# Kernel tuning notes

Hardware: AMD Instinct MI355X
Metric: run time of the kernel (lower is better)

The kernel has to match this reference:

```python
import jax, jax.numpy as jnp
import numpy as np

NUM_HEADS = 8
N_WIN = 7
TOPK = 4


def _grid2seq(x, rs, m):
    # x: (B, C, H, W) -> (B, m, nregion, reg_size, head_dim)
    B, C, H, W = x.shape
    rh, rw = H // rs[0], W // rs[1]
    d = C // m
    x = x.reshape(B, m, d, rh, rs[0], rw, rs[1])
    x = jnp.einsum('bmdhpwq->bmhwpqd', x).reshape(B, m, rh * rw, rs[0] * rs[1], d)
    return x, rh, rw


def _seq2grid(x, rh, rw, rs):
    B, m, nreg, rsq, d = x.shape
    x = x.reshape(B, m, rh, rw, rs[0], rs[1], d)
    return jnp.einsum('bmhwpqd->bmdhpwq', x).reshape(B, m * d, rh * rs[0], rw * rs[1])


def setup_inputs() -> dict:
    key = jax.random.key(0)
    ks = jax.random.split(key, 7)
    C = 256
    inp = {
        'x': jax.random.normal(ks[0], (16, C, 56, 56), jnp.float32),
        'w_qkv': jax.random.normal(ks[1], (3 * C, C), jnp.float32) * 0.02,
        'b_qkv': jax.random.normal(ks[2], (3 * C,), jnp.float32) * 0.02,
        'w_lepe': jax.random.normal(ks[3], (C, 1, 3, 3), jnp.float32) * 0.02,
        'b_lepe': jax.random.normal(ks[4], (C,), jnp.float32) * 0.02,
        'w_out': jax.random.normal(ks[5], (C, C), jnp.float32) * 0.02,
        'b_out': jax.random.normal(ks[6], (C,), jnp.float32) * 0.02,
    }
    return inp


def reference(x, w_qkv, b_qkv, w_lepe, b_lepe, w_out, b_out):
    N, C, H, W = x.shape
    m = NUM_HEADS
    d = C // m
    scale = d ** (-0.5)
    rs = (max(1, H // N_WIN), max(1, W // N_WIN))  # (8, 8) here; H,W divisible -> no pad
    rh, rw = H // rs[0], W // rs[1]

    # 1x1 conv qkv projection
    qkv = jnp.einsum('nchw,oc->nohw', x, w_qkv) + b_qkv[None, :, None, None]
    q, k, v = jnp.split(qkv, 3, axis=1)

    # region-level routing (avg_pool over each region; exact divisibility -> plain mean)
    def region_mean(t):
        return t.reshape(N, C, rh, rs[0], rw, rs[1]).mean(axis=(3, 5))  # (N,C,rh,rw)

    q_r = jax.lax.stop_gradient(region_mean(q)).reshape(N, C, rh * rw).transpose(0, 2, 1)  # (N,nreg,C)
    k_r = jax.lax.stop_gradient(region_mean(k)).reshape(N, C, rh * rw)  # (N,C,nreg)
    a_r = q_r @ k_r  # (N, nreg, nreg)
    k_fixed = min(TOPK, a_r.shape[-1])
    _, idx_r = jax.lax.top_k(a_r, k_fixed)  # (N, nreg, topk)
    idx_r = jnp.broadcast_to(idx_r[:, None], (N, m, rh * rw, k_fixed))  # (N,m,nreg,topk)

    # token-level attention within routed regions
    q_seq, _, _ = _grid2seq(q, rs, m)  # (N,m,nreg,rs2,d)
    k_seq, _, _ = _grid2seq(k, rs, m)
    v_seq, _, _ = _grid2seq(v, rs, m)
    rs2 = k_seq.shape[-2]

    gather = jax.vmap(jax.vmap(lambda seq, i: seq[i]))  # over (batch, head)
    key_g = gather(k_seq, idx_r).reshape(N, m, rh * rw, k_fixed * rs2, d)
    val_g = gather(v_seq, idx_r).reshape(N, m, rh * rw, k_fixed * rs2, d)

    attn = jax.nn.softmax(jnp.einsum('bmnpd,bmnkd->bmnpk', q_seq * scale, key_g), axis=-1)
    out = jnp.einsum('bmnpk,bmnkd->bmnpd', attn, val_g)
    out = _seq2grid(out, rh, rw, rs)  # (N, C, H, W)

    # LEPE: depthwise 3x3 conv on v
    lepe = jax.lax.conv_general_dilated(
        v, w_lepe, window_strides=(1, 1), padding='SAME',
        feature_group_count=C, dimension_numbers=('NCHW', 'OIHW', 'NCHW'))
    out = out + lepe + b_lepe[None, :, None, None]

    # 1x1 conv output projection
    out = jnp.einsum('nchw,oc->nohw', out, w_out) + b_out[None, :, None, None]
    return out
```

## Files before the change

kernel.cpp:

```cpp
#include <hip/hip_runtime.h>
#include <cstdint>

#define DEV __device__ __forceinline__

using short8 = __attribute__((ext_vector_type(8))) short;
using f32x4  = __attribute__((ext_vector_type(4))) float;

#define MFMA __builtin_amdgcn_mfma_f32_16x16x32_bf16

DEV float bf2f(unsigned short u){
  union { unsigned int i; float f; } v; v.i = ((unsigned int)u) << 16; return v.f;
}
DEV unsigned short f2bf(float f){
  union { float f; unsigned int i; } v; v.f = f;
  unsigned int x = v.i;
  return (unsigned short)((x + 0x7fffu + ((x >> 16) & 1u)) >> 16);
}
DEV unsigned int cvtpk(float a, float b){
  unsigned int r;
  asm("v_cvt_pk_bf16_f32 %0, %1, %2" : "=v"(r) : "v"(a), "v"(b));
  return r;
}

__global__ __launch_bounds__(256) void k_prep(const float* __restrict__ w_qkv,
                                              const float* __restrict__ w_out,
                                              unsigned short* __restrict__ wqh_t,
                                              unsigned short* __restrict__ woh_t,
                                              unsigned short* __restrict__ wol_t){
  int i = blockIdx.x*256 + threadIdx.x;
  if (i < 196608){
    int o = i >> 8, c = i & 255, kc = c >> 5, kk = c & 31;
    wqh_t[kc*24576 + o*32 + kk] = f2bf(w_qkv[i]);
  } else {
    int j = i - 196608;
    if (j < 65536){
      int o = j >> 8, c = j & 255, kc = c >> 5, kk = c & 31;
      float v = w_out[j];
      unsigned short h = f2bf(v);
      int dst = kc*8192 + o*32 + kk;
      woh_t[dst] = h;
      wol_t[dst] = f2bf(v - bf2f(h));
    }
  }
}

__global__ __launch_bounds__(256) void k_xbar(const float* __restrict__ x,
                                              float* __restrict__ xbar){
  const int ry = blockIdx.x, n = blockIdx.y, cz = blockIdx.z;
  const int t = threadIdx.x, cg = t>>6, lane = t&63;
  for (int ci = 0; ci < 16; ++ci){
    int c = cz*64 + ci*4 + cg;
    const float* base = x + ((size_t)n*256 + c)*3136 + ry*8*56;
    float acc = 0.f;
    if (lane < 56){
      #pragma unroll
      for (int yy = 0; yy < 8; ++yy) acc += base[yy*56 + lane];
    }
    acc += __shfl_xor(acc, 1, 64);
    acc += __shfl_xor(acc, 2, 64);
    acc += __shfl_xor(acc, 4, 64);
    if ((lane&7) == 0 && lane < 56)
      xbar[((size_t)n*49 + ry*7 + (lane>>3))*256 + c] = acc * (1.0f/64.0f);
  }
}

__global__ __launch_bounds__(256) void k_qrkr(const float* __restrict__ xbar,
                                              const float* __restrict__ w_qkv,
                                              const float* __restrict__ b_qkv,
                                              float* __restrict__ q_r,
                                              float* __restrict__ k_r){
  __shared__ float4 xb4[448];
  const int wb = blockIdx.x, n = blockIdx.y, rz = blockIdx.z, t = threadIdx.x;
  {
    const float4* src = (const float4*)(xbar + (size_t)n*12544) + rz*448;
    for (int i = t; i < 448; i += 256) xb4[i] = src[i];
  }
  const int wrow = wb*64 + (t>>2), kl = t&3;
  float4 wreg[16];
  {
    const float4* wsrc = (const float4*)(w_qkv + (size_t)wrow*256) + kl*16;
    #pragma unroll
    for (int i = 0; i < 16; ++i) wreg[i] = wsrc[i];
  }
  __syncthreads();
  const float bias = b_qkv[wrow];
  for (int rl = 0; rl < 7; ++rl){
    float s = 0.f;
    #pragma unroll
    for (int i = 0; i < 16; ++i){
      float4 a = wreg[i], b = xb4[rl*64 + kl*16 + i];
      s += a.x*b.x + a.y*b.y + a.z*b.z + a.w*b.w;
    }
    s += __shfl_xor(s, 1, 64);
    s += __shfl_xor(s, 2, 64);
    if (kl == 0){
      int reg = rz*7 + rl;
      if (wrow < 256) q_r[((size_t)n*49 + reg)*256 + wrow] = s + bias;
      else            k_r[((size_t)n*49 + reg)*256 + wrow - 256] = s + bias;
    }
  }
}

__global__ __launch_bounds__(64) void k_topk(const float* __restrict__ q_r,
                                             const float* __restrict__ k_r,
                                             int* __restrict__ idx){
  __shared__ float sc[49];
  const int qreg = blockIdx.x, n = blockIdx.y, l = threadIdx.x;
  const float* qrow = q_r + ((size_t)n*49 + qreg)*256;
  const float q0 = qrow[l], q1 = qrow[l+64], q2 = qrow[l+128], q3 = qrow[l+192];
  for (int kr = 0; kr < 49; ++kr){
    const float* krow = k_r + ((size_t)n*49 + kr)*256;
    float s = q0*krow[l] + q1*krow[l+64] + q2*krow[l+128] + q3*krow[l+192];
    #pragma unroll
    for (int m = 1; m < 64; m <<= 1) s += __shfl_xor(s, m, 64);
    if (l == 0) sc[kr] = s;
  }
  __syncthreads();
  if (l == 0){
    #pragma unroll
    for (int s = 0; s < 4; ++s){
      float best = -3.4e38f; int bi = 0;
      for (int kr = 0; kr < 49; ++kr) if (sc[kr] > best){ best = sc[kr]; bi = kr; }
      idx[((size_t)n*49 + qreg)*4 + s] = bi;
      sc[bi] = -3.4e38f;
    }
  }
}

__global__ __launch_bounds__(256) void k_qkv(const float* __restrict__ x,
                                             const unsigned short* __restrict__ wqh_t,
                                             const float* __restrict__ b_qkv,
                                             unsigned short* __restrict__ q_rm,
                                             unsigned short* __restrict__ k_rm,
                                             unsigned short* __restrict__ v_t){
  __shared__ unsigned short xl[64*256];
  const int lin = blockIdx.x;
  const int xcd = lin & 7, jj = lin >> 3;
  const int jobid = xcd*294 + jj;
  const int z = jobid % 3;
  const int pair = jobid / 3;
  const int reg = pair % 49, n = pair / 49;

  const int ry = reg/7, rx = reg%7;
  const int t = threadIdx.x, w = t>>6, g = (t>>4)&3, c16 = t&15;
  {
    const int pq = (t & 15)*4, cc = t >> 4;
    const int row = pq >> 3, col = pq & 7;
    const float* src = x + ((size_t)n*256 + cc)*3136 + (ry*8 + row)*56 + rx*8 + col;
    for (int ci = 0; ci < 16; ++ci){
      float4 v4 = *reinterpret_cast<const float4*>(src + (size_t)ci*16*3136);
      int c = ci*16 + cc;
      xl[((pq+0)*256 + c) ^ (((pq+0)&15)<<3)] = f2bf(v4.x);
      xl[((pq+1)*256 + c) ^ (((pq+1)&15)<<3)] = f2bf(v4.y);
      xl[((pq+2)*256 + c) ^ (((pq+2)&15)<<3)] = f2bf(v4.z);
      xl[((pq+3)*256 + c) ^ (((pq+3)&15)<<3)] = f2bf(v4.w);
    }
  }
  __syncthreads();
  const size_t rb = (size_t)(n*8)*49 + reg;
  const int osw = w*16;

  if (z < 2){
    f32x4 acc[4][4] = {};
    for (int kc = 0; kc < 8; ++kc){
      short8 xf[4];
      #pragma unroll
      for (int pt = 0; pt < 4; ++pt){
        int p = pt*16 + c16;
        xf[pt] = *reinterpret_cast<const short8*>(&xl[(p*256 + kc*32 + 8*g) ^ ((p&15)<<3)]);
      }
      #pragma unroll
      for (int oi = 0; oi < 4; ++oi){
        const int os = z*256 + oi*64 + osw;
        short8 wf = *reinterpret_cast<const short8*>(wqh_t + (size_t)kc*24576 + (os + c16)*32 + 8*g);
        #pragma unroll
        for (int pt = 0; pt < 4; ++pt)
          acc[oi][pt] = MFMA(xf[pt], wf, acc[oi][pt], 0, 0, 0);
      }
    }
    #pragma unroll
    for (int oi = 0; oi < 4; ++oi){
      const int o = z*256 + oi*64 + osw + c16;
      const float bias = b_qkv[o];
      const int oc = o & 255, hh = oc >> 5, dd = oc & 31;
      unsigned short* dst = ((z == 0) ? q_rm : k_rm) + (rb + hh*49)*2048 + dd;
      #pragma unroll
      for (int pt = 0; pt < 4; ++pt)
        #pragma unroll
        for (int r = 0; r < 4; ++r){
          int tok = pt*16 + 4*g + r;
          dst[tok*32] = f2bf(acc[oi][pt][r] + bias);
        }
    }
  } else {
    f32x4 acc[4][4] = {};
    for (int kc = 0; kc < 8; ++kc){
      short8 xf[4];
      #pragma unroll
      for (int pt = 0; pt < 4; ++pt){
        int p = pt*16 + c16;
        xf[pt] = *reinterpret_cast<const short8*>(&xl[(p*256 + kc*32 + 8*g) ^ ((p&15)<<3)]);
      }
      #pragma unroll
      for (int oi = 0; oi < 4; ++oi){
        const int os = oi*64 + osw;
        short8 wf = *reinterpret_cast<const short8*>(wqh_t + (size_t)kc*24576 + (512 + os + c16)*32 + 8*g);
        #pragma unroll
        for (int pt = 0; pt < 4; ++pt)
          acc[oi][pt] = MFMA(wf, xf[pt], acc[oi][pt], 0, 0, 0);
      }
    }
    #pragma unroll
    for (int oi = 0; oi < 4; ++oi){
      #pragma unroll
      for (int r = 0; r < 4; ++r){
        int c = oi*64 + osw + 4*g + r;
        const float bias = b_qkv[512 + c];
        int hh = c >> 5, ch = c & 31;
        unsigned short* dst = v_t + (rb + hh*49)*2048 + ch*32;
        #pragma unroll
        for (int pt = 0; pt < 4; ++pt){
          int tok = pt*16 + c16;
          dst[(tok>>5)*1024 + (tok&31)] = f2bf(acc[oi][pt][r] + bias);
        }
      }
    }
  }
}

__global__ __launch_bounds__(256, 4) void k_attn(const unsigned short* __restrict__ q_rm,
                                                 const unsigned short* __restrict__ k_rm,
                                                 const unsigned short* __restrict__ v_t,
                                                 const int* __restrict__ idx,
                                                 const float* __restrict__ w_lepe,
                                                 const float* __restrict__ b_lepe,
                                                 unsigned short* __restrict__ att_hi,
                                                 unsigned short* __restrict__ att_lo){
  __shared__ unsigned short Pw[4*2048];
  __shared__ unsigned short halo[10*320];
  __shared__ float wl_s[288];
  __shared__ float bl_s[32];

  const int lin = blockIdx.x + 49*(blockIdx.y + 8*blockIdx.z);
  const int xcd = lin & 7, j = lin >> 3;
  const int jq = j / 49;
  const int qreg = j - jq*49;
  const int hn = jq*8 + xcd;
  const int h = hn & 7, n = hn >> 3;

  const int t = threadIdx.x, w = t>>6, g = (t>>4)&3, c16 = t&15;
  const int ry = qreg/7, rx = qreg%7;
  const int gy0 = ry*8;

  int4 ridx = *reinterpret_cast<const int4*>(idx + ((size_t)n*49 + qreg)*4);
  int regs[4] = {ridx.x, ridx.y, ridx.z, ridx.w};

  const size_t hb = ((size_t)(n*8 + h))*49;

  wl_s[t < 288 ? t : 0] = w_lepe[h*288 + (t < 288 ? t : 0)];
  if (t < 32){
    wl_s[256 + t] = w_lepe[h*288 + 256 + t];
    bl_s[t] = b_lepe[h*32 + t];
  }
  #pragma unroll
  for (int pass = 0; pass < 2; ++pass){
    int s = pass ? (256 + t) : t;
    if (pass == 0 || t < 64){
      const int dy = s >> 5, c = s & 31;
      const int yy = gy0 + dy - 1;
      short8 inner = {0,0,0,0,0,0,0,0};
      unsigned short eL = 0, eR = 0;
      if (yy >= 0 && yy < 56){
        const int iry = yy >> 3, y7 = yy & 7;
        const size_t rowb = (size_t)(y7>>2)*1024 + c*32 + (y7&3)*8;
        inner = *reinterpret_cast<const short8*>(v_t + (hb + iry*7 + rx)*2048 + rowb);
        if (rx > 0) eL = v_t[(hb + iry*7 + rx - 1)*2048 + rowb + 7];
        if (rx < 6) eR = v_t[(hb + iry*7 + rx + 1)*2048 + rowb];
      }
      unsigned short* drow = &halo[dy*320 + c*10];
      drow[0] = eL;
      #pragma unroll
      for (int jj2 = 0; jj2 < 8; ++jj2) drow[1 + jj2] = (unsigned short)inner[jj2];
      drow[9] = eR;
    }
  }

  const int qtok = w*16 + c16;
  short8 qf = *reinterpret_cast<const short8*>(q_rm + (hb + qreg)*2048 + qtok*32 + 8*g);

  f32x4 s_acc[16];
  #pragma unroll
  for (int f = 0; f < 16; ++f){
    const int tt = (f&3)*16 + c16;
    short8 kf = *reinterpret_cast<const short8*>(
        k_rm + (hb + regs[f>>2])*2048 + tt*32 + 8*g);
    f32x4 z = {0.f, 0.f, 0.f, 0.f};
    s_acc[f] = MFMA(qf, kf, z, 0, 0, 0);
  }

  const float scale2 = 0.1767766952966369f * 1.4426950408889634f;
  float inv[4];
  #pragma unroll
  for (int r = 0; r < 4; ++r){
    float m = -3.4e38f;
    #pragma unroll
    for (int f = 0; f < 16; ++f) m = fmaxf(m, s_acc[f][r]);
    #pragma unroll
    for (int d = 1; d < 16; d <<= 1) m = fmaxf(m, __shfl_xor(m, d, 64));
    const float nms = -m*scale2;
    float su = 0.f;
    #pragma unroll
    for (int f = 0; f < 16; ++f){
      float e = exp2f(fmaf(s_acc[f][r], scale2, nms));
      s_acc[f][r] = e; su += e;
    }
    #pragma unroll
    for (int d = 1; d < 16; d <<= 1) su += __shfl_xor(su, d, 64);
    inv[r] = __builtin_amdgcn_rcpf(su);
  }

  f32x4 oacc[2] = {};
  unsigned short* wb2 = &Pw[w*2048];
  #pragma unroll
  for (int h2 = 0; h2 < 2; ++h2){
    #pragma unroll
    for (int r = 0; r < 4; ++r){
      int q = 4*g + r;
      #pragma unroll
      for (int f2 = 0; f2 < 8; f2 += 2){
        unsigned int pk = cvtpk(s_acc[8*h2 + f2][r], s_acc[8*h2 + f2 + 1][r]);
        wb2[(q*128 + f2*16 + c16) ^ ((q&7)<<3)]     = (unsigned short)pk;
        wb2[(q*128 + (f2+1)*16 + c16) ^ ((q&7)<<3)] = (unsigned short)(pk >> 16);
      }
    }
    asm volatile("s_waitcnt lgkmcnt(0)" ::: "memory");
    __builtin_amdgcn_sched_barrier(0);
    #pragma unroll
    for (int tcl = 0; tcl < 4; ++tcl){
      const int tc = 4*h2 + tcl;
      short8 pf = *reinterpret_cast<const short8*>(&wb2[(c16*128 + tcl*32 + 8*g) ^ ((c16&7)<<3)]);
      const size_t vb = (hb + regs[tc>>1])*2048 + (tc&1)*1024 + 8*g;
      #pragma unroll
      for (int dt = 0; dt < 2; ++dt){
        short8 vf = *reinterpret_cast<const short8*>(v_t + vb + (dt*16 + c16)*32);
        oacc[dt] = MFMA(pf, vf, oacc[dt], 0, 0, 0);
      }
    }
  }

  __syncthreads();
  const int tok0 = w*16 + 4*g;
  const int ty = tok0>>3, tx0 = tok0&7;
  #pragma unroll
  for (int dt = 0; dt < 2; ++dt){
    const int cl = dt*16 + c16;
    float wl[9];
    #pragma unroll
    for (int kk = 0; kk < 9; ++kk) wl[kk] = wl_s[cl*9 + kk];
    const float bl = bl_s[cl];
    float vwin[3][6];
    #pragma unroll
    for (int dy = 0; dy < 3; ++dy){
      const unsigned short* hrow = &halo[(ty+dy)*320 + cl*10 + tx0];
      #pragma unroll
      for (int jj = 0; jj < 6; ++jj)
        vwin[dy][jj] = bf2f(hrow[jj]);
    }
    #pragma unroll
    for (int r = 0; r < 4; ++r){
      float a = fmaf(oacc[dt][r], inv[r], bl);
      #pragma unroll
      for (int dy = 0; dy < 3; ++dy)
        #pragma unroll
        for (int dx = 0; dx < 3; ++dx)
          a += wl[dy*3 + dx] * vwin[dy][r + dx];
      int tok = tok0 + r;
      size_t o = ((size_t)(n*49 + qreg)*8 + h)*2048 + tok*32 + dt*16 + c16;
      unsigned short hi = (unsigned short)cvtpk(a, a);
      att_hi[o] = hi;
      float alo = a - bf2f(hi);
      att_lo[o] = (unsigned short)cvtpk(alo, alo);
    }
  }
}

__global__ __launch_bounds__(512) void k_oproj(const unsigned short* __restrict__ ah_,
                                               const unsigned short* __restrict__ al_,
                                               const unsigned short* __restrict__ wh_t,
                                               const unsigned short* __restrict__ wl_t,
                                               const float* __restrict__ b_out,
                                               float* __restrict__ out){
  const int reg = blockIdx.x, n = blockIdx.y;
  const int t = threadIdx.x, w8 = t>>6, g = (t>>4)&3, c16 = t&15;
  const int ry = reg/7, rx = reg%7;
  const size_t abase = ((size_t)(n*49 + reg))*8*2048;
  const int os1 = w8*16, os2 = os1 + 128;
  f32x4 acc[2][4] = {};
  for (int kc = 0; kc < 8; ++kc){
    const size_t wb = (size_t)kc*8192 + 8*g;
    short8 wh1 = *reinterpret_cast<const short8*>(wh_t + wb + (os1 + c16)*32);
    short8 wl1 = *reinterpret_cast<const short8*>(wl_t + wb + (os1 + c16)*32);
    short8 wh2 = *reinterpret_cast<const short8*>(wh_t + wb + (os2 + c16)*32);
    short8 wl2 = *reinterpret_cast<const short8*>(wl_t + wb + (os2 + c16)*32);
    #pragma unroll
    for (int pt = 0; pt < 4; ++pt){
      size_t off = abase + (size_t)kc*2048 + (pt*16 + c16)*32 + 8*g;
      short8 xh = *reinterpret_cast<const short8*>(ah_ + off);
      short8 xl = *reinterpret_cast<const short8*>(al_ + off);
      acc[0][pt] = MFMA(wh1, xh, acc[0][pt], 0, 0, 0);
      acc[0][pt] = MFMA(wh1, xl, acc[0][pt], 0, 0, 0);
      acc[0][pt] = MFMA(wl1, xh, acc[0][pt], 0, 0, 0);
      acc[1][pt] = MFMA(wh2, xh, acc[1][pt], 0, 0, 0);
      acc[1][pt] = MFMA(wh2, xl, acc[1][pt], 0, 0, 0);
      acc[1][pt] = MFMA(wl2, xh, acc[1][pt], 0, 0, 0);
    }
  }
  #pragma unroll
  for (int s = 0; s < 2; ++s){
    const int os = s ? os2 : os1;
    #pragma unroll
    for (int r = 0; r < 4; ++r){
      int o = os + 4*g + r;
      float bias = b_out[o];
      #pragma unroll
      for (int pt = 0; pt < 4; ++pt){
        int tok = pt*16 + c16;
        int p = (ry*8 + (tok>>3))*56 + rx*8 + (tok&7);
        out[((size_t)n*256 + o)*3136 + p] = acc[s][pt][r] + bias;
      }
    }
  }
}

extern "C" void kernel_launch(void* const* d_in, const int* in_sizes, int n_in,
                              void* d_out, int out_size, void* d_ws, size_t ws_size,
                              hipStream_t stream){
  const float* x      = (const float*)d_in[0];
  const float* w_qkv  = (const float*)d_in[1];
  const float* b_qkv  = (const float*)d_in[2];
  const float* w_lepe = (const float*)d_in[3];
  const float* b_lepe = (const float*)d_in[4];
  const float* w_out  = (const float*)d_in[5];
  const float* b_out  = (const float*)d_in[6];
  float* out = (float*)d_out;

  char* ws = (char*)d_ws;
  size_t off = 0;
  auto take = [&](size_t bytes)->char*{
    char* p = ws + off; off += (bytes + 255) & ~(size_t)255; return p;
  };
  const size_t TEN = (size_t)16*3136*256*2;
  unsigned short* q_rm   = (unsigned short*)take(TEN);
  unsigned short* k_rm   = (unsigned short*)take(TEN);
  unsigned short* v_t    = (unsigned short*)take(TEN);
  unsigned short* att_hi = (unsigned short*)take(TEN);
  unsigned short* att_lo = (unsigned short*)take(TEN);
  float* xbar = (float*)take((size_t)16*49*256*4);
  float* q_r  = (float*)take((size_t)16*49*256*4);
  float* k_r  = (float*)take((size_t)16*49*256*4);
  int*   idxb = (int*)take((size_t)16*49*4*4);
  unsigned short* wqh_t = (unsigned short*)take((size_t)768*256*2);
  unsigned short* woh_t = (unsigned short*)take((size_t)256*256*2);
  unsigned short* wol_t = (unsigned short*)take((size_t)256*256*2);

  k_prep <<<dim3(1024), 256, 0, stream>>>(w_qkv, w_out, wqh_t, woh_t, wol_t);
  k_xbar <<<dim3(7, 16, 4), 256, 0, stream>>>(x, xbar);
  k_qrkr <<<dim3(8, 16, 7), 256, 0, stream>>>(xbar, w_qkv, b_qkv, q_r, k_r);
  k_topk <<<dim3(49, 16), 64, 0, stream>>>(q_r, k_r, idxb);
  k_qkv  <<<dim3(2352), 256, 0, stream>>>(x, wqh_t, b_qkv, q_rm, k_rm, v_t);
  k_attn <<<dim3(49, 8, 16), 256, 0, stream>>>(q_rm, k_rm, v_t, idxb, w_lepe, b_lepe, att_hi, att_lo);
  k_oproj<<<dim3(49, 16), 512, 0, stream>>>(att_hi, att_lo, woh_t, wol_t, b_out, out);
}
```

Before: 253.0 us.

## Transpose QK^T MFMA and pass P through cross-lane shuffles instead of LDS

Swaps the MFMA operands so each lane holds scores for a single query row, which reduces the softmax max/sum reductions to two cross-lane shuffles per lane. The probabilities are then repacked into the A-operand layout of the PV MFMA with bpermute-style shuffles and selects, removing the per-wave LDS staging buffer and its waitcnt barriers. This cuts LDS use, which could raise occupancy. In exchange it adds many shuffle instructions and extra shuffles to redistribute the reciprocal sums.

Measured after the change: 250.4 us. About the same (-1.0%).

```diff
diff --git a/kernel.cpp b/kernel.cpp
--- a/kernel.cpp
+++ b/kernel.cpp
@@ -236,7 +236,6 @@
                                                  const float* __restrict__ b_lepe,
                                                  unsigned short* __restrict__ att_hi,
                                                  unsigned short* __restrict__ att_lo){
-  __shared__ unsigned short Pw[4*2048];
   __shared__ unsigned short halo[10*320];
   __shared__ float wl_s[288];
   __shared__ float bl_s[32];
@@ -295,58 +294,62 @@
     short8 kf = *reinterpret_cast<const short8*>(
         k_rm + (hb + regs[f>>2])*2048 + tt*32 + 8*g);
     f32x4 z = {0.f, 0.f, 0.f, 0.f};
-    s_acc[f] = MFMA(qf, kf, z, 0, 0, 0);
+    s_acc[f] = MFMA(kf, qf, z, 0, 0, 0);
   }
 
   const float scale2 = 0.1767766952966369f * 1.4426950408889634f;
-  float inv[4];
-  #pragma unroll
-  for (int r = 0; r < 4; ++r){
-    float m = -3.4e38f;
-    #pragma unroll
-    for (int f = 0; f < 16; ++f) m = fmaxf(m, s_acc[f][r]);
-    #pragma unroll
-    for (int d = 1; d < 16; d <<= 1) m = fmaxf(m, __shfl_xor(m, d, 64));
-    const float nms = -m*scale2;
-    float su = 0.f;
-    #pragma unroll
-    for (int f = 0; f < 16; ++f){
+  float m = -3.4e38f;
+  #pragma unroll
+  for (int f = 0; f < 16; ++f)
+    #pragma unroll
+    for (int r = 0; r < 4; ++r) m = fmaxf(m, s_acc[f][r]);
+  m = fmaxf(m, __shfl_xor(m, 16, 64));
+  m = fmaxf(m, __shfl_xor(m, 32, 64));
+  const float nms = -m*scale2;
+  float su = 0.f;
+  #pragma unroll
+  for (int f = 0; f < 16; ++f)
+    #pragma unroll
+    for (int r = 0; r < 4; ++r){
       float e = exp2f(fmaf(s_acc[f][r], scale2, nms));
       s_acc[f][r] = e; su += e;
     }
-    #pragma unroll
-    for (int d = 1; d < 16; d <<= 1) su += __shfl_xor(su, d, 64);
-    inv[r] = __builtin_amdgcn_rcpf(su);
-  }
+  su += __shfl_xor(su, 16, 64);
+  su += __shfl_xor(su, 32, 64);
+  const float inv_lane = __builtin_amdgcn_rcpf(su);
 
   f32x4 oacc[2] = {};
-  unsigned short* wb2 = &Pw[w*2048];
-  #pragma unroll
-  for (int h2 = 0; h2 < 2; ++h2){
-    #pragma unroll
-    for (int r = 0; r < 4; ++r){
-      int q = 4*g + r;
-      #pragma unroll
-      for (int f2 = 0; f2 < 8; f2 += 2){
-        unsigned int pk = cvtpk(s_acc[8*h2 + f2][r], s_acc[8*h2 + f2 + 1][r]);
-        wb2[(q*128 + f2*16 + c16) ^ ((q&7)<<3)]     = (unsigned short)pk;
-        wb2[(q*128 + (f2+1)*16 + c16) ^ ((q&7)<<3)] = (unsigned short)(pk >> 16);
-      }
-    }
-    asm volatile("s_waitcnt lgkmcnt(0)" ::: "memory");
-    __builtin_amdgcn_sched_barrier(0);
-    #pragma unroll
-    for (int tcl = 0; tcl < 4; ++tcl){
-      const int tc = 4*h2 + tcl;
-      short8 pf = *reinterpret_cast<const short8*>(&wb2[(c16*128 + tcl*32 + 8*g) ^ ((c16&7)<<3)]);
-      const size_t vb = (hb + regs[tc>>1])*2048 + (tc&1)*1024 + 8*g;
-      #pragma unroll
-      for (int dt = 0; dt < 2; ++dt){
-        short8 vf = *reinterpret_cast<const short8*>(v_t + vb + (dt*16 + c16)*32);
-        oacc[dt] = MFMA(pf, vf, oacc[dt], 0, 0, 0);
-      }
-    }
-  }
+  const int srcA = (t & 15) | ((t & 16) << 1);
+  const int srcB = srcA + 16;
+  const bool gsel = (t & 32) != 0;
+  #pragma unroll
+  for (int tc = 0; tc < 8; ++tc){
+    const int fb = (tc>>1)*4 + (tc&1)*2;
+    unsigned int a0 = cvtpk(s_acc[fb][0],   s_acc[fb][1]);
+    unsigned int a1 = cvtpk(s_acc[fb][2],   s_acc[fb][3]);
+    unsigned int b0 = cvtpk(s_acc[fb+1][0], s_acc[fb+1][1]);
+    unsigned int b1 = cvtpk(s_acc[fb+1][2], s_acc[fb+1][3]);
+    unsigned int wa0 = __shfl((int)a0, srcA, 64), wa1 = __shfl((int)a1, srcA, 64);
+    unsigned int wa2 = __shfl((int)a0, srcB, 64), wa3 = __shfl((int)a1, srcB, 64);
+    unsigned int wb0 = __shfl((int)b0, srcA, 64), wb1 = __shfl((int)b1, srcA, 64);
+    unsigned int wb2 = __shfl((int)b0, srcB, 64), wb3 = __shfl((int)b1, srcB, 64);
+    union { unsigned int u[4]; short8 s8; } pfu;
+    pfu.u[0] = gsel ? wb0 : wa0;
+    pfu.u[1] = gsel ? wb1 : wa1;
+    pfu.u[2] = gsel ? wb2 : wa2;
+    pfu.u[3] = gsel ? wb3 : wa3;
+    const size_t vb = (hb + regs[tc>>1])*2048 + (tc&1)*1024 + 8*g;
+    #pragma unroll
+    for (int dt = 0; dt < 2; ++dt){
+      short8 vf = *reinterpret_cast<const short8*>(v_t + vb + (dt*16 + c16)*32);
+      oacc[dt] = MFMA(pfu.s8, vf, oacc[dt], 0, 0, 0);
+    }
+  }
+
+  float invq[4];
+  #pragma unroll
+  for (int r = 0; r < 4; ++r)
+    invq[r] = __shfl(inv_lane, 4*g + r, 64);
 
   __syncthreads();
   const int tok0 = w*16 + 4*g;
@@ -368,7 +371,7 @@
     }
     #pragma unroll
     for (int r = 0; r < 4; ++r){
-      float a = fmaf(oacc[dt][r], inv[r], bl);
+      float a = fmaf(oacc[dt][r], invq[r], bl);
       #pragma unroll
       for (int dy = 0; dy < 3; ++dy)
         #pragma unroll
```
